# Kernel tuning notes

Hardware: AMD Instinct MI355X
Metric: run time of the kernel (lower is better)

The kernel has to match this reference:

```python
import jax, jax.numpy as jnp
import numpy as np

N0, N1, F, H = 30000, 6000, 1024, 512
E00, E01, E10, E11 = 600000, 300000, 300000, 400000


def setup_inputs() -> dict:
    key = jax.random.key(0)
    keys = iter(jax.random.split(key, 64))

    def randn(shape, s=1.0):
        return jax.random.normal(next(keys), shape, dtype=jnp.float32) * s

    inp = {"feat0": randn((N0, F)), "feat1": randn((N1, F))}
    adj_specs = {"a00": (N0, N0, E00), "a01": (N0, N1, E01),
                 "a10": (N1, N0, E10), "a11a": (N1, N1, E11), "a11b": (N1, N1, E11)}
    for name, (ni, nj, e) in adj_specs.items():
        inp[name + "_row"] = jax.random.randint(next(keys), (e,), 0, ni, dtype=jnp.int32)
        inp[name + "_col"] = jax.random.randint(next(keys), (e,), 0, nj, dtype=jnp.int32)
        inp[name + "_val"] = jax.random.uniform(next(keys), (e,), dtype=jnp.float32)
    for rel in ["00", "01", "10", "11a", "11b"]:
        inp["W1_" + rel] = randn((F, H), 0.02)
        inp["W2_" + rel] = randn((H, H), 0.05)
        inp["W3_" + rel] = randn((H, H), 0.05)
    return inp


def _spmm(row, col, val, x, n_out):
    # sparse adjacency (n_out x n_in) @ x, COO edge-list form
    return jax.ops.segment_sum(val[:, None] * x[col], row, num_segments=n_out)


def reference(feat0, feat1,
              a00_row, a00_col, a00_val, a01_row, a01_col, a01_val,
              a10_row, a10_col, a10_val, a11a_row, a11a_col, a11a_val,
              a11b_row, a11b_col, a11b_val,
              W1_00, W1_01, W1_10, W1_11a, W1_11b,
              W2_00, W2_01, W2_10, W2_11a, W2_11b,
              W3_00, W3_01, W3_10, W3_11a, W3_11b):
    relu = jax.nn.relu

    def conv(row, col, val, x, W, n_out):
        # GraphConvolution(Sparse)Multi with identity act: adj @ (x @ W)
        return _spmm(row, col, val, x @ W, n_out)

    # Layer 1: relu(add_n over (i, j) edge types)
    e0_0 = relu(conv(a00_row, a00_col, a00_val, feat0, W1_00, N0)
                + conv(a01_row, a01_col, a01_val, feat1, W1_01, N0))
    e0_1 = relu(conv(a10_row, a10_col, a10_val, feat0, W1_10, N1)
                + conv(a11a_row, a11a_col, a11a_val, feat1, W1_11a, N1)
                + conv(a11b_row, a11b_col, a11b_val, feat1, W1_11b, N1))

    # Layer 2: original does embeddings1 = embeddings0 + embeddings1 (python list
    # concat), so embeddings1[j] == embeddings0[j] -> layer-2 inputs are e0.
    e2_0 = relu(conv(a00_row, a00_col, a00_val, e0_0, W2_00, N0)
                + conv(a01_row, a01_col, a01_val, e0_1, W2_01, N0))
    e2_1 = relu(conv(a10_row, a10_col, a10_val, e0_0, W2_10, N1)
                + conv(a11a_row, a11a_col, a11a_val, e0_1, W2_11a, N1)
                + conv(a11b_row, a11b_col, a11b_val, e0_1, W2_11b, N1))

    # Layer 3: inputs are layer-2 outputs (same list-concat quirk); no relu.
    e3_0 = (conv(a00_row, a00_col, a00_val, e2_0, W3_00, N0)
            + conv(a01_row, a01_col, a01_val, e2_1, W3_01, N0))
    e3_1 = (conv(a10_row, a10_col, a10_val, e2_0, W3_10, N1)
            + conv(a11a_row, a11a_col, a11a_val, e2_1, W3_11a, N1)
            + conv(a11b_row, a11b_col, a11b_val, e2_1, W3_11b, N1))

    # Final: concat([e0, embeddings1(=e0), e3]) per object type; stack obj types
    # along node axis for a single output array.
    out0 = jnp.concatenate([e0_0, e0_0, e3_0], axis=1)  # [N0, 3H]
    out1 = jnp.concatenate([e0_1, e0_1, e3_1], axis=1)  # [N1, 3H]
    return jnp.concatenate([out0, out1], axis=0)  # [N0+N1, 3H]
```

## Files before the change

kernel.cpp:

```cpp
#include <hip/hip_runtime.h>
#include <stdint.h>

#define N0 30000
#define N1 6000
#define FDIM 1024
#define HDIM 512
#define E00 600000
#define E01 300000
#define E10 300000
#define E11A 400000
#define E11B 400000
#define NE_TOT (E00 + E01 + E10 + E11A + E11B)

typedef __attribute__((ext_vector_type(4))) float f32x4;
typedef __attribute__((ext_vector_type(8))) __bf16 bf16x8;

__device__ __forceinline__ unsigned short f2bf(float f) {
  unsigned u = __float_as_uint(f);
  u += 0x7fffu + ((u >> 16) & 1u);
  return (unsigned short)(u >> 16);
}

__device__ __forceinline__ void gload16(const void* g, void* l) {
  __builtin_amdgcn_global_load_lds((const __attribute__((address_space(1))) void*)g,
                                   (__attribute__((address_space(3))) void*)l, 16, 0, 0);
}

__global__ void conv_bf16_kernel(const float* __restrict__ src, unsigned short* __restrict__ dst, int n4) {
  int gid = blockIdx.x * blockDim.x + threadIdx.x;
  if (gid >= n4) return;
  float4 v = ((const float4*)src)[gid];
  ushort4 o;
  o.x = f2bf(v.x); o.y = f2bf(v.y); o.z = f2bf(v.z); o.w = f2bf(v.w);
  ((ushort4*)dst)[gid] = o;
}

__global__ void conv_weights_kernel(const float* __restrict__ w00, const float* __restrict__ w10,
                                    const float* __restrict__ w01, const float* __restrict__ w11a,
                                    const float* __restrict__ w11b,
                                    unsigned short* __restrict__ dst0, unsigned short* __restrict__ dst1, int K) {
  int gid = blockIdx.x * blockDim.x + threadIdx.x;
  int total0 = 1024 * K;
  int total1 = 1536 * K;
  if (gid < total0) {
    int n = gid / K, k = gid - n * K;
    const float* w = (n < 512) ? w00 : w10;
    int nn = n & 511;
    dst0[gid] = f2bf(w[(size_t)k * 512 + nn]);
  } else if (gid < total0 + total1) {
    int g = gid - total0;
    int n = g / K, k = g - n * K;
    const float* w = (n < 512) ? w01 : ((n < 1024) ? w11a : w11b);
    int nn = n & 511;
    dst1[g] = f2bf(w[(size_t)k * 512 + nn]);
  }
}

__global__ void zero_ints(int* p, int n) {
  int g = blockIdx.x * blockDim.x + threadIdx.x;
  if (g < n) p[g] = 0;
}

__global__ void hist5(const int* __restrict__ r0, const int* __restrict__ r1, const int* __restrict__ r2,
                      const int* __restrict__ r3, const int* __restrict__ r4,
                      int* c0, int* c1, int* c2, int* c3, int* c4) {
  int g = blockIdx.x * blockDim.x + threadIdx.x;
  const int* r; int* c; int e;
  if (g < E00) { r = r0; c = c0; e = g; }
  else if (g < E00 + E01) { r = r1; c = c1; e = g - E00; }
  else if (g < E00 + E01 + E10) { r = r2; c = c2; e = g - (E00 + E01); }
  else if (g < E00 + E01 + E10 + E11A) { r = r3; c = c3; e = g - (E00 + E01 + E10); }
  else if (g < NE_TOT) { r = r4; c = c4; e = g - (E00 + E01 + E10 + E11A); }
  else return;
  atomicAdd(&c[r[e]], 1);
}

__global__ __launch_bounds__(1024) void scan5p(int* c0, int* rp0, int* c1, int* rp1,
                                               int* c2, int* rp2, int* c3, int* rp3,
                                               int* c4, int* rp4) {
  int b = blockIdx.x;
  int* cnt; int* rp; int n;
  if (b == 0) { cnt = c0; rp = rp0; n = N0; }
  else if (b == 1) { cnt = c1; rp = rp1; n = N0; }
  else if (b == 2) { cnt = c2; rp = rp2; n = N1; }
  else if (b == 3) { cnt = c3; rp = rp3; n = N1; }
  else { cnt = c4; rp = rp4; n = N1; }
  __shared__ int wsum[16];
  const int tid = threadIdx.x, lane = tid & 63, w = tid >> 6;
  int carry = 0;
  for (int base = 0; base < n; base += 1024) {
    int i = base + tid;
    int v = (i < n) ? cnt[i] : 0;
    int x = v;
    #pragma unroll
    for (int d = 1; d < 64; d <<= 1) {
      int y = __shfl_up(x, d, 64);
      if (lane >= d) x += y;
    }
    if (lane == 63) wsum[w] = x;
    __syncthreads();
    if (w == 0) {
      int t = (lane < 16) ? wsum[lane] : 0;
      #pragma unroll
      for (int d = 1; d < 16; d <<= 1) {
        int y = __shfl_up(t, d, 64);
        if (lane >= d) t += y;
      }
      if (lane < 16) wsum[lane] = t;
    }
    __syncthreads();
    int wpref = (w > 0) ? wsum[w - 1] : 0;
    int excl = carry + wpref + (x - v);
    if (i < n) { rp[i] = excl; cnt[i] = excl; }
    carry += wsum[15];
    __syncthreads();
  }
  if (tid == 0) rp[n] = carry;
}

__global__ void scatter5(const int* __restrict__ r0, const int* __restrict__ q0, const float* __restrict__ v0,
                         int* cur0, int* sc0, float* sv0,
                         const int* __restrict__ r1, const int* __restrict__ q1, const float* __restrict__ v1,
                         int* cur1, int* sc1, float* sv1,
                         const int* __restrict__ r2, const int* __restrict__ q2, const float* __restrict__ v2,
                         int* cur2, int* sc2, float* sv2,
                         const int* __restrict__ r3, const int* __restrict__ q3, const float* __restrict__ v3,
                         int* cur3, int* sc3, float* sv3,
                         const int* __restrict__ r4, const int* __restrict__ q4, const float* __restrict__ v4,
                         int* cur4, int* sc4, float* sv4) {
  int g = blockIdx.x * blockDim.x + threadIdx.x;
  const int* r; const int* q; const float* v; int* cur; int* sc; float* sv; int e;
  if (g < E00) { r = r0; q = q0; v = v0; cur = cur0; sc = sc0; sv = sv0; e = g; }
  else if (g < E00 + E01) { r = r1; q = q1; v = v1; cur = cur1; sc = sc1; sv = sv1; e = g - E00; }
  else if (g < E00 + E01 + E10) { r = r2; q = q2; v = v2; cur = cur2; sc = sc2; sv = sv2; e = g - (E00 + E01); }
  else if (g < E00 + E01 + E10 + E11A) { r = r3; q = q3; v = v3; cur = cur3; sc = sc3; sv = sv3; e = g - (E00 + E01 + E10); }
  else if (g < NE_TOT) { r = r4; q = q4; v = v4; cur = cur4; sc = sc4; sv = sv4; e = g - (E00 + E01 + E10 + E11A); }
  else return;
  int row = r[e];
  int p = atomicAdd(&cur[row], 1);
  sc[p] = q[e];
  sv[p] = v[e];
}

#define BM 128
#define BN 128
#define BK 64

__global__ __launch_bounds__(256) void gemm_bf16(const unsigned short* __restrict__ A,
                                                 const unsigned short* __restrict__ Bt,
                                                 unsigned short* __restrict__ C,
                                                 int M, int N, int K, int nbx) {
  __shared__ unsigned short As[BM * BK];
  __shared__ unsigned short Bs[BN * BK];
  const int nwg = gridDim.x;
  const int orig = blockIdx.x;
  const int q = nwg >> 3, rr = nwg & 7;
  const int xcd = orig & 7, pos = orig >> 3;
  const int wg = (xcd < rr ? xcd * (q + 1) : rr * (q + 1) + (xcd - rr) * q) + pos;
  const int bx = wg % nbx;
  const int by = wg / nbx;

  const int tid = threadIdx.x;
  const int lane = tid & 63;
  const int wid = tid >> 6;
  const int m0 = bx * BM;
  const int n0 = by * BN;
  const int wm = (wid >> 1) * 64;
  const int wn = (wid & 1) * 64;

  f32x4 acc[4][4] = {};

  const int srow = wid * 32 + (lane >> 3);
  const int scol = (lane & 7) * 8;

  for (int k0 = 0; k0 < K; k0 += BK) {
    #pragma unroll
    for (int c = 0; c < 4; ++c) {
      int gr = m0 + srow + c * 8;
      if (gr > M - 1) gr = M - 1;
      gload16(A + (size_t)gr * K + k0 + scol, As + (wid * 32 + c * 8) * BK);
      int gn = n0 + srow + c * 8;
      gload16(Bt + (size_t)gn * K + k0 + scol, Bs + (wid * 32 + c * 8) * BK);
    }
    __syncthreads();
    #pragma unroll
    for (int ks = 0; ks < 2; ++ks) {
      bf16x8 af[4], bfr[4];
      #pragma unroll
      for (int i = 0; i < 4; i++)
        af[i] = *(const bf16x8*)(As + (wm + i * 16 + (lane & 15)) * BK + ks * 32 + (lane >> 4) * 8);
      #pragma unroll
      for (int j = 0; j < 4; j++)
        bfr[j] = *(const bf16x8*)(Bs + (wn + j * 16 + (lane & 15)) * BK + ks * 32 + (lane >> 4) * 8);
      #pragma unroll
      for (int i = 0; i < 4; i++)
        #pragma unroll
        for (int j = 0; j < 4; j++)
          acc[i][j] = __builtin_amdgcn_mfma_f32_16x16x32_bf16(af[i], bfr[j], acc[i][j], 0, 0, 0);
    }
    __syncthreads();
  }

  #pragma unroll
  for (int i = 0; i < 4; i++) {
    int rbase = m0 + wm + i * 16 + (lane >> 4) * 4;
    #pragma unroll
    for (int j = 0; j < 4; j++) {
      int col = n0 + wn + j * 16 + (lane & 15);
      #pragma unroll
      for (int r = 0; r < 4; r++) {
        int row = rbase + r;
        if (row < M) C[(size_t)row * N + col] = f2bf(acc[i][j][r]);
      }
    }
  }
}

__device__ __forceinline__ void acc8(float* acc, float v, uint4 u) {
  acc[0] += v * __uint_as_float(u.x << 16);
  acc[1] += v * __uint_as_float(u.x & 0xffff0000u);
  acc[2] += v * __uint_as_float(u.y << 16);
  acc[3] += v * __uint_as_float(u.y & 0xffff0000u);
  acc[4] += v * __uint_as_float(u.z << 16);
  acc[5] += v * __uint_as_float(u.z & 0xffff0000u);
  acc[6] += v * __uint_as_float(u.w << 16);
  acc[7] += v * __uint_as_float(u.w & 0xffff0000u);
}

__global__ __launch_bounds__(256) void spmm_kernel(
    int nrows, int nseg,
    const int* __restrict__ rp0, const int* __restrict__ ci0, const float* __restrict__ cv0,
    const unsigned short* __restrict__ g0, int ld0, int off0,
    const int* __restrict__ rp1, const int* __restrict__ ci1, const float* __restrict__ cv1,
    const unsigned short* __restrict__ g1, int ld1, int off1,
    const int* __restrict__ rp2, const int* __restrict__ ci2, const float* __restrict__ cv2,
    const unsigned short* __restrict__ g2, int ld2, int off2,
    int do_relu,
    unsigned short* __restrict__ ebf,
    float* __restrict__ outp, int out_row0, int out_col0, int dup) {
  const int lane = threadIdx.x & 63;
  const int r = blockIdx.x * 4 + (threadIdx.x >> 6);
  if (r >= nrows) return;
  float acc[8] = {0.f, 0.f, 0.f, 0.f, 0.f, 0.f, 0.f, 0.f};
  for (int s = 0; s < nseg; ++s) {
    const int* rp; const int* ci; const float* cv; const unsigned short* g; int ld, off;
    if (s == 0) { rp = rp0; ci = ci0; cv = cv0; g = g0; ld = ld0; off = off0; }
    else if (s == 1) { rp = rp1; ci = ci1; cv = cv1; g = g1; ld = ld1; off = off1; }
    else { rp = rp2; ci = ci2; cv = cv2; g = g2; ld = ld2; off = off2; }
    const unsigned short* gb = g + off + lane * 8;
    int e = rp[r], e1 = rp[r + 1];
    for (; e + 3 < e1; e += 4) {
      int ca = ci[e], cb = ci[e + 1], cc = ci[e + 2], cd = ci[e + 3];
      float va = cv[e], vb = cv[e + 1], vc = cv[e + 2], vd = cv[e + 3];
      uint4 ua = *(const uint4*)(gb + (size_t)ca * ld);
      uint4 ub = *(const uint4*)(gb + (size_t)cb * ld);
      uint4 uc = *(const uint4*)(gb + (size_t)cc * ld);
      uint4 ud = *(const uint4*)(gb + (size_t)cd * ld);
      acc8(acc, va, ua); acc8(acc, vb, ub); acc8(acc, vc, uc); acc8(acc, vd, ud);
    }
    for (; e < e1; ++e) {
      int c = ci[e];
      float v = cv[e];
      uint4 u = *(const uint4*)(gb + (size_t)c * ld);
      acc8(acc, v, u);
    }
  }
  if (do_relu) {
    #pragma unroll
    for (int i = 0; i < 8; i++) acc[i] = fmaxf(acc[i], 0.f);
  }
  if (ebf) {
    uint4 o;
    o.x = (unsigned)f2bf(acc[0]) | ((unsigned)f2bf(acc[1]) << 16);
    o.y = (unsigned)f2bf(acc[2]) | ((unsigned)f2bf(acc[3]) << 16);
    o.z = (unsigned)f2bf(acc[4]) | ((unsigned)f2bf(acc[5]) << 16);
    o.w = (unsigned)f2bf(acc[6]) | ((unsigned)f2bf(acc[7]) << 16);
    *(uint4*)(ebf + (size_t)r * HDIM + lane * 8) = o;
  }
  if (outp) {
    float4 v0; v0.x = acc[0]; v0.y = acc[1]; v0.z = acc[2]; v0.w = acc[3];
    float4 v1; v1.x = acc[4]; v1.y = acc[5]; v1.z = acc[6]; v1.w = acc[7];
    size_t base = (size_t)(out_row0 + r) * 1536 + out_col0 + lane * 8;
    *(float4*)(outp + base) = v0;
    *(float4*)(outp + base + 4) = v1;
    if (dup) {
      *(float4*)(outp + base + 512) = v0;
      *(float4*)(outp + base + 516) = v1;
    }
  }
}

extern "C" void kernel_launch(void* const* d_in, const int* in_sizes, int n_in,
                              void* d_out, int out_size, void* d_ws, size_t ws_size,
                              hipStream_t stream) {
  const float* feat0 = (const float*)d_in[0];
  const float* feat1 = (const float*)d_in[1];
  const int* a00_row = (const int*)d_in[2];
  const int* a00_col = (const int*)d_in[3];
  const float* a00_val = (const float*)d_in[4];
  const int* a01_row = (const int*)d_in[5];
  const int* a01_col = (const int*)d_in[6];
  const float* a01_val = (const float*)d_in[7];
  const int* a10_row = (const int*)d_in[8];
  const int* a10_col = (const int*)d_in[9];
  const float* a10_val = (const float*)d_in[10];
  const int* a11a_row = (const int*)d_in[11];
  const int* a11a_col = (const int*)d_in[12];
  const float* a11a_val = (const float*)d_in[13];
  const int* a11b_row = (const int*)d_in[14];
  const int* a11b_col = (const int*)d_in[15];
  const float* a11b_val = (const float*)d_in[16];

  const float *W1[5], *W2[5], *W3[5];
  if (in_sizes[18] == 512 * 512) {
    for (int r = 0; r < 5; r++) {
      W1[r] = (const float*)d_in[17 + 3 * r];
      W2[r] = (const float*)d_in[18 + 3 * r];
      W3[r] = (const float*)d_in[19 + 3 * r];
    }
  } else {
    for (int r = 0; r < 5; r++) {
      W1[r] = (const float*)d_in[17 + r];
      W2[r] = (const float*)d_in[22 + r];
      W3[r] = (const float*)d_in[27 + r];
    }
  }

  char* ws = (char*)d_ws;
  size_t off = 0;
  auto alloc = [&](size_t bytes) -> char* {
    char* p = ws + off;
    off += (bytes + 255) & ~(size_t)255;
    return p;
  };
  unsigned short* feat0b = (unsigned short*)alloc((size_t)N0 * FDIM * 2);
  unsigned short* feat1b = (unsigned short*)alloc((size_t)N1 * FDIM * 2);
  unsigned short* Wt1_0 = (unsigned short*)alloc((size_t)1024 * 1024 * 2);
  unsigned short* Wt1_1 = (unsigned short*)alloc((size_t)1536 * 1024 * 2);
  unsigned short* Wt2_0 = (unsigned short*)alloc((size_t)1024 * 512 * 2);
  unsigned short* Wt2_1 = (unsigned short*)alloc((size_t)1536 * 512 * 2);
  unsigned short* Wt3_0 = (unsigned short*)alloc((size_t)1024 * 512 * 2);
  unsigned short* Wt3_1 = (unsigned short*)alloc((size_t)1536 * 512 * 2);
  unsigned short* G0 = (unsigned short*)alloc((size_t)N0 * 1024 * 2);
  unsigned short* G1 = (unsigned short*)alloc((size_t)N1 * 1536 * 2);
  unsigned short* e0_0 = (unsigned short*)alloc((size_t)N0 * HDIM * 2);
  unsigned short* e0_1 = (unsigned short*)alloc((size_t)N1 * HDIM * 2);
  int* cur = (int*)alloc((size_t)(2 * N0 + 3 * N1) * 4);
  int* cur00 = cur;
  int* cur01 = cur + N0;
  int* cur10 = cur + 2 * N0;
  int* cur11a = cur + 2 * N0 + N1;
  int* cur11b = cur + 2 * N0 + 2 * N1;
  int* rp00 = (int*)alloc((N0 + 1) * 4);
  int* rp01 = (int*)alloc((N0 + 1) * 4);
  int* rp10 = (int*)alloc((N1 + 1) * 4);
  int* rp11a = (int*)alloc((N1 + 1) * 4);
  int* rp11b = (int*)alloc((N1 + 1) * 4);
  int* sc00 = (int*)alloc((size_t)E00 * 4);
  float* sv00 = (float*)alloc((size_t)E00 * 4);
  int* sc01 = (int*)alloc((size_t)E01 * 4);
  float* sv01 = (float*)alloc((size_t)E01 * 4);
  int* sc10 = (int*)alloc((size_t)E10 * 4);
  float* sv10 = (float*)alloc((size_t)E10 * 4);
  int* sc11a = (int*)alloc((size_t)E11A * 4);
  float* sv11a = (float*)alloc((size_t)E11A * 4);
  int* sc11b = (int*)alloc((size_t)E11B * 4);
  float* sv11b = (float*)alloc((size_t)E11B * 4);
  unsigned short* e2_0 = feat0b;
  unsigned short* e2_1 = feat1b;
  float* out = (float*)d_out;

  conv_bf16_kernel<<<(N0 * FDIM / 4 + 255) / 256, 256, 0, stream>>>(feat0, feat0b, N0 * FDIM / 4);
  conv_bf16_kernel<<<(N1 * FDIM / 4 + 255) / 256, 256, 0, stream>>>(feat1, feat1b, N1 * FDIM / 4);
  conv_weights_kernel<<<(2560 * 1024 + 255) / 256, 256, 0, stream>>>(W1[0], W1[2], W1[1], W1[3], W1[4], Wt1_0, Wt1_1, 1024);
  conv_weights_kernel<<<(2560 * 512 + 255) / 256, 256, 0, stream>>>(W2[0], W2[2], W2[1], W2[3], W2[4], Wt2_0, Wt2_1, 512);
  conv_weights_kernel<<<(2560 * 512 + 255) / 256, 256, 0, stream>>>(W3[0], W3[2], W3[1], W3[3], W3[4], Wt3_0, Wt3_1, 512);

  int ncur = 2 * N0 + 3 * N1;
  zero_ints<<<(ncur + 255) / 256, 256, 0, stream>>>(cur, ncur);
  hist5<<<(NE_TOT + 255) / 256, 256, 0, stream>>>(a00_row, a01_row, a10_row, a11a_row, a11b_row,
                                                  cur00, cur01, cur10, cur11a, cur11b);
  scan5p<<<5, 1024, 0, stream>>>(cur00, rp00, cur01, rp01, cur10, rp10, cur11a, rp11a, cur11b, rp11b);
  scatter5<<<(NE_TOT + 255) / 256, 256, 0, stream>>>(
      a00_row, a00_col, a00_val, cur00, sc00, sv00,
      a01_row, a01_col, a01_val, cur01, sc01, sv01,
      a10_row, a10_col, a10_val, cur10, sc10, sv10,
      a11a_row, a11a_col, a11a_val, cur11a, sc11a, sv11a,
      a11b_row, a11b_col, a11b_val, cur11b, sc11b, sv11b);

  dim3 blk(256);
  int nbx0 = (N0 + BM - 1) / BM;
  int nbx1 = (N1 + BM - 1) / BM;
  dim3 g0a(nbx0 * (1024 / BN));
  dim3 g0b(nbx1 * (1536 / BN));

  gemm_bf16<<<g0a, blk, 0, stream>>>(feat0b, Wt1_0, G0, N0, 1024, 1024, nbx0);
  gemm_bf16<<<g0b, blk, 0, stream>>>(feat1b, Wt1_1, G1, N1, 1536, 1024, nbx1);
  spmm_kernel<<<(N0 + 3) / 4, blk, 0, stream>>>(N0, 2,
      rp00, sc00, sv00, G0, 1024, 0,
      rp01, sc01, sv01, G1, 1536, 0,
      nullptr, nullptr, nullptr, nullptr, 0, 0,
      1, e0_0, out, 0, 0, 1);
  spmm_kernel<<<(N1 + 3) / 4, blk, 0, stream>>>(N1, 3,
      rp10, sc10, sv10, G0, 1024, 512,
      rp11a, sc11a, sv11a, G1, 1536, 512,
      rp11b, sc11b, sv11b, G1, 1536, 1024,
      1, e0_1, out, N0, 0, 1);

  gemm_bf16<<<g0a, blk, 0, stream>>>(e0_0, Wt2_0, G0, N0, 1024, 512, nbx0);
  gemm_bf16<<<g0b, blk, 0, stream>>>(e0_1, Wt2_1, G1, N1, 1536, 512, nbx1);
  spmm_kernel<<<(N0 + 3) / 4, blk, 0, stream>>>(N0, 2,
      rp00, sc00, sv00, G0, 1024, 0,
      rp01, sc01, sv01, G1, 1536, 0,
      nullptr, nullptr, nullptr, nullptr, 0, 0,
      1, e2_0, nullptr, 0, 0, 0);
  spmm_kernel<<<(N1 + 3) / 4, blk, 0, stream>>>(N1, 3,
      rp10, sc10, sv10, G0, 1024, 512,
      rp11a, sc11a, sv11a, G1, 1536, 512,
      rp11b, sc11b, sv11b, G1, 1536, 1024,
      1, e2_1, nullptr, 0, 0, 0);

  gemm_bf16<<<g0a, blk, 0, stream>>>(e2_0, Wt3_0, G0, N0, 1024, 512, nbx0);
  gemm_bf16<<<g0b, blk, 0, stream>>>(e2_1, Wt3_1, G1, N1, 1536, 512, nbx1);
  spmm_kernel<<<(N0 + 3) / 4, blk, 0, stream>>>(N0, 2,
      rp00, sc00, sv00, G0, 1024, 0,
      rp01, sc01, sv01, G1, 1536, 0,
      nullptr, nullptr, nullptr, nullptr, 0, 0,
      0, nullptr, out, 0, 1024, 0);
  spmm_kernel<<<(N1 + 3) / 4, blk, 0, stream>>>(N1, 3,
      rp10, sc10, sv10, G0, 1024, 512,
      rp11a, sc11a, sv11a, G1, 1536, 512,
      rp11b, sc11b, sv11b, G1, 1536, 1024,
      0, nullptr, out, N0, 1024, 0);
}
```

Before: 1.347 ms.

## Reorder layers 2-3 to aggregate first, then multiply by concatenated weights

Layers 2 and 3 now compute (A·X) first for each relation, writing the aggregated features side by side into a wide buffer, and then run one GEMM with K-concatenated weights (K=1024 or 1536, N=512). This replaces the earlier (X·W) then SpMM order. The SpMM now gathers 512-wide rows instead of slices of 1024/1536-wide rows, and the per-relation sums fold into the GEMM's K reduction. ReLU and the fp32 output write are fused into the GEMM epilogue. The gather loop is also unrolled to 8 edges, and row bounds are made wave-uniform with readfirstlane.

```diff
diff --git a/kernel.cpp b/kernel.cpp
--- a/kernel.cpp
+++ b/kernel.cpp
@@ -53,6 +53,25 @@
     const float* w = (n < 512) ? w01 : ((n < 1024) ? w11a : w11b);
     int nn = n & 511;
     dst1[g] = f2bf(w[(size_t)k * 512 + nn]);
+  }
+}
+
+__global__ void conv_wk_kernel(const float* __restrict__ w00, const float* __restrict__ w01,
+                               const float* __restrict__ w10, const float* __restrict__ w11a,
+                               const float* __restrict__ w11b,
+                               unsigned short* __restrict__ dst0, unsigned short* __restrict__ dst1) {
+  int gid = blockIdx.x * blockDim.x + threadIdx.x;
+  const int T0 = 512 * 1024;
+  const int T1 = 512 * 1536;
+  if (gid < T0) {
+    int n = gid >> 10, k = gid & 1023;
+    const float* w = (k < 512) ? w00 : w01;
+    dst0[gid] = f2bf(w[(size_t)(k & 511) * 512 + n]);
+  } else if (gid < T0 + T1) {
+    int g = gid - T0;
+    int n = g / 1536, k = g - n * 1536;
+    const float* w = (k < 512) ? w10 : ((k < 1024) ? w11a : w11b);
+    dst1[g] = f2bf(w[(size_t)(k & 511) * 512 + n]);
   }
 }
 
@@ -146,10 +165,11 @@
 #define BN 128
 #define BK 64
 
+template<int MODE>
 __global__ __launch_bounds__(256) void gemm_bf16(const unsigned short* __restrict__ A,
                                                  const unsigned short* __restrict__ Bt,
-                                                 unsigned short* __restrict__ C,
-                                                 int M, int N, int K, int nbx) {
+                                                 void* __restrict__ Cv,
+                                                 int M, int N, int K, int nbx, int ldc) {
   __shared__ unsigned short As[BM * BK];
   __shared__ unsigned short Bs[BN * BK];
   const int nwg = gridDim.x;
@@ -210,13 +230,18 @@
       #pragma unroll
       for (int r = 0; r < 4; r++) {
         int row = rbase + r;
-        if (row < M) C[(size_t)row * N + col] = f2bf(acc[i][j][r]);
+        if (row < M) {
+          float v = acc[i][j][r];
+          if (MODE == 1) v = fmaxf(v, 0.f);
+          if (MODE == 2) ((float*)Cv)[(size_t)row * ldc + col] = v;
+          else ((unsigned short*)Cv)[(size_t)row * ldc + col] = f2bf(v);
+        }
       }
     }
   }
 }
 
-__device__ __forceinline__ void acc8(float* acc, float v, uint4 u) {
+__device__ __forceinline__ void acc8(float* acc, float v, const uint4& u) {
   acc[0] += v * __uint_as_float(u.x << 16);
   acc[1] += v * __uint_as_float(u.x & 0xffff0000u);
   acc[2] += v * __uint_as_float(u.y << 16);
@@ -227,6 +252,33 @@
   acc[7] += v * __uint_as_float(u.w & 0xffff0000u);
 }
 
+__device__ __forceinline__ void gather_row(const int* __restrict__ ci, const float* __restrict__ cv,
+                                           const unsigned short* __restrict__ gb, int ld,
+                                           int e, int e1, float* acc) {
+  for (; e + 7 < e1; e += 8) {
+    int c0 = ci[e], c1 = ci[e + 1], c2 = ci[e + 2], c3 = ci[e + 3];
+    int c4 = ci[e + 4], c5 = ci[e + 5], c6 = ci[e + 6], c7 = ci[e + 7];
+    float v0 = cv[e], v1 = cv[e + 1], v2 = cv[e + 2], v3 = cv[e + 3];
+    float v4 = cv[e + 4], v5 = cv[e + 5], v6 = cv[e + 6], v7 = cv[e + 7];
+    uint4 u0 = *(const uint4*)(gb + (size_t)c0 * ld);
+    uint4 u1 = *(const uint4*)(gb + (size_t)c1 * ld);
+    uint4 u2 = *(const uint4*)(gb + (size_t)c2 * ld);
+    uint4 u3 = *(const uint4*)(gb + (size_t)c3 * ld);
+    uint4 u4 = *(const uint4*)(gb + (size_t)c4 * ld);
+    uint4 u5 = *(const uint4*)(gb + (size_t)c5 * ld);
+    uint4 u6 = *(const uint4*)(gb + (size_t)c6 * ld);
+    uint4 u7 = *(const uint4*)(gb + (size_t)c7 * ld);
+    acc8(acc, v0, u0); acc8(acc, v1, u1); acc8(acc, v2, u2); acc8(acc, v3, u3);
+    acc8(acc, v4, u4); acc8(acc, v5, u5); acc8(acc, v6, u6); acc8(acc, v7, u7);
+  }
+  for (; e < e1; ++e) {
+    int c = ci[e];
+    float v = cv[e];
+    uint4 u = *(const uint4*)(gb + (size_t)c * ld);
+    acc8(acc, v, u);
+  }
+}
+
 __global__ __launch_bounds__(256) void spmm_kernel(
     int nrows, int nseg,
     const int* __restrict__ rp0, const int* __restrict__ ci0, const float* __restrict__ cv0,
@@ -235,9 +287,8 @@
     const unsigned short* __restrict__ g1, int ld1, int off1,
     const int* __restrict__ rp2, const int* __restrict__ ci2, const float* __restrict__ cv2,
     const unsigned short* __restrict__ g2, int ld2, int off2,
-    int do_relu,
     unsigned short* __restrict__ ebf,
-    float* __restrict__ outp, int out_row0, int out_col0, int dup) {
+    float* __restrict__ outp, int out_row0) {
   const int lane = threadIdx.x & 63;
   const int r = blockIdx.x * 4 + (threadIdx.x >> 6);
   if (r >= nrows) return;
@@ -247,46 +298,54 @@
     if (s == 0) { rp = rp0; ci = ci0; cv = cv0; g = g0; ld = ld0; off = off0; }
     else if (s == 1) { rp = rp1; ci = ci1; cv = cv1; g = g1; ld = ld1; off = off1; }
     else { rp = rp2; ci = ci2; cv = cv2; g = g2; ld = ld2; off = off2; }
-    const unsigned short* gb = g + off + lane * 8;
-    int e = rp[r], e1 = rp[r + 1];
-    for (; e + 3 < e1; e += 4) {
-      int ca = ci[e], cb = ci[e + 1], cc = ci[e + 2], cd = ci[e + 3];
-      float va = cv[e], vb = cv[e + 1], vc = cv[e + 2], vd = cv[e + 3];
-      uint4 ua = *(const uint4*)(gb + (size_t)ca * ld);
-      uint4 ub = *(const uint4*)(gb + (size_t)cb * ld);
-      uint4 uc = *(const uint4*)(gb + (size_t)cc * ld);
-      uint4 ud = *(const uint4*)(gb + (size_t)cd * ld);
-      acc8(acc, va, ua); acc8(acc, vb, ub); acc8(acc, vc, uc); acc8(acc, vd, ud);
-    }
-    for (; e < e1; ++e) {
-      int c = ci[e];
-      float v = cv[e];
-      uint4 u = *(const uint4*)(gb + (size_t)c * ld);
-      acc8(acc, v, u);
-    }
-  }
-  if (do_relu) {
-    #pragma unroll
-    for (int i = 0; i < 8; i++) acc[i] = fmaxf(acc[i], 0.f);
-  }
-  if (ebf) {
+    int e = __builtin_amdgcn_readfirstlane(rp[r]);
+    int e1 = __builtin_amdgcn_readfirstlane(rp[r + 1]);
+    gather_row(ci, cv, g + off + lane * 8, ld, e, e1, acc);
+  }
+  #pragma unroll
+  for (int i = 0; i < 8; i++) acc[i] = fmaxf(acc[i], 0.f);
+  uint4 o;
+  o.x = (unsigned)f2bf(acc[0]) | ((unsigned)f2bf(acc[1]) << 16);
+  o.y = (unsigned)f2bf(acc[2]) | ((unsigned)f2bf(acc[3]) << 16);
+  o.z = (unsigned)f2bf(acc[4]) | ((unsigned)f2bf(acc[5]) << 16);
+  o.w = (unsigned)f2bf(acc[6]) | ((unsigned)f2bf(acc[7]) << 16);
+  *(uint4*)(ebf + (size_t)r * HDIM + lane * 8) = o;
+  float4 v0; v0.x = acc[0]; v0.y = acc[1]; v0.z = acc[2]; v0.w = acc[3];
+  float4 v1; v1.x = acc[4]; v1.y = acc[5]; v1.z = acc[6]; v1.w = acc[7];
+  size_t base = (size_t)(out_row0 + r) * 1536 + lane * 8;
+  *(float4*)(outp + base) = v0;
+  *(float4*)(outp + base + 4) = v1;
+  *(float4*)(outp + base + 512) = v0;
+  *(float4*)(outp + base + 516) = v1;
+}
+
+__global__ __launch_bounds__(256) void spmm_sep(
+    int nrows, int nseg,
+    const int* __restrict__ rp0, const int* __restrict__ ci0, const float* __restrict__ cv0,
+    const unsigned short* __restrict__ t0,
+    const int* __restrict__ rp1, const int* __restrict__ ci1, const float* __restrict__ cv1,
+    const unsigned short* __restrict__ t1,
+    const int* __restrict__ rp2, const int* __restrict__ ci2, const float* __restrict__ cv2,
+    const unsigned short* __restrict__ t2,
+    unsigned short* __restrict__ outp, int ld_out) {
+  const int lane = threadIdx.x & 63;
+  const int r = blockIdx.x * 4 + (threadIdx.x >> 6);
+  if (r >= nrows) return;
+  for (int s = 0; s < nseg; ++s) {
+    const int* rp; const int* ci; const float* cv; const unsigned short* t;
+    if (s == 0) { rp = rp0; ci = ci0; cv = cv0; t = t0; }
+    else if (s == 1) { rp = rp1; ci = ci1; cv = cv1; t = t1; }
+    else { rp = rp2; ci = ci2; cv = cv2; t = t2; }
+    float acc[8] = {0.f, 0.f, 0.f, 0.f, 0.f, 0.f, 0.f, 0.f};
+    int e = __builtin_amdgcn_readfirstlane(rp[r]);
+    int e1 = __builtin_amdgcn_readfirstlane(rp[r + 1]);
+    gather_row(ci, cv, t + lane * 8, HDIM, e, e1, acc);
     uint4 o;
     o.x = (unsigned)f2bf(acc[0]) | ((unsigned)f2bf(acc[1]) << 16);
     o.y = (unsigned)f2bf(acc[2]) | ((unsigned)f2bf(acc[3]) << 16);
     o.z = (unsigned)f2bf(acc[4]) | ((unsigned)f2bf(acc[5]) << 16);
     o.w = (unsigned)f2bf(acc[6]) | ((unsigned)f2bf(acc[7]) << 16);
-    *(uint4*)(ebf + (size_t)r * HDIM + lane * 8) = o;
-  }
-  if (outp) {
-    float4 v0; v0.x = acc[0]; v0.y = acc[1]; v0.z = acc[2]; v0.w = acc[3];
-    float4 v1; v1.x = acc[4]; v1.y = acc[5]; v1.z = acc[6]; v1.w = acc[7];
-    size_t base = (size_t)(out_row0 + r) * 1536 + out_col0 + lane * 8;
-    *(float4*)(outp + base) = v0;
-    *(float4*)(outp + base + 4) = v1;
-    if (dup) {
-      *(float4*)(outp + base + 512) = v0;
-      *(float4*)(outp + base + 516) = v1;
-    }
+    *(uint4*)(outp + (size_t)r * ld_out + s * HDIM + lane * 8) = o;
   }
 }
 
@@ -337,10 +396,10 @@
   unsigned short* feat1b = (unsigned short*)alloc((size_t)N1 * FDIM * 2);
   unsigned short* Wt1_0 = (unsigned short*)alloc((size_t)1024 * 1024 * 2);
   unsigned short* Wt1_1 = (unsigned short*)alloc((size_t)1536 * 1024 * 2);
-  unsigned short* Wt2_0 = (unsigned short*)alloc((size_t)1024 * 512 * 2);
-  unsigned short* Wt2_1 = (unsigned short*)alloc((size_t)1536 * 512 * 2);
-  unsigned short* Wt3_0 = (unsigned short*)alloc((size_t)1024 * 512 * 2);
-  unsigned short* Wt3_1 = (unsigned short*)alloc((size_t)1536 * 512 * 2);
+  unsigned short* Wt2_0 = (unsigned short*)alloc((size_t)512 * 1024 * 2);
+  unsigned short* Wt2_1 = (unsigned short*)alloc((size_t)512 * 1536 * 2);
+  unsigned short* Wt3_0 = (unsigned short*)alloc((size_t)512 * 1024 * 2);
+  unsigned short* Wt3_1 = (unsigned short*)alloc((size_t)512 * 1536 * 2);
   unsigned short* G0 = (unsigned short*)alloc((size_t)N0 * 1024 * 2);
   unsigned short* G1 = (unsigned short*)alloc((size_t)N1 * 1536 * 2);
   unsigned short* e0_0 = (unsigned short*)alloc((size_t)N0 * HDIM * 2);
@@ -373,8 +432,8 @@
   conv_bf16_kernel<<<(N0 * FDIM / 4 + 255) / 256, 256, 0, stream>>>(feat0, feat0b, N0 * FDIM / 4);
   conv_bf16_kernel<<<(N1 * FDIM / 4 + 255) / 256, 256, 0, stream>>>(feat1, feat1b, N1 * FDIM / 4);
   conv_weights_kernel<<<(2560 * 1024 + 255) / 256, 256, 0, stream>>>(W1[0], W1[2], W1[1], W1[3], W1[4], Wt1_0, Wt1_1, 1024);
-  conv_weights_kernel<<<(2560 * 512 + 255) / 256, 256, 0, stream>>>(W2[0], W2[2], W2[1], W2[3], W2[4], Wt2_0, Wt2_1, 512);
-  conv_weights_kernel<<<(2560 * 512 + 255) / 256, 256, 0, stream>>>(W3[0], W3[2], W3[1], W3[3], W3[4], Wt3_0, Wt3_1, 512);
+  conv_wk_kernel<<<(512 * 2560 + 255) / 256, 256, 0, stream>>>(W2[0], W2[1], W2[2], W2[3], W2[4], Wt2_0, Wt2_1);
+  conv_wk_kernel<<<(512 * 2560 + 255) / 256, 256, 0, stream>>>(W3[0], W3[1], W3[2], W3[3], W3[4], Wt3_0, Wt3_1);
 
   int ncur = 2 * N0 + 3 * N1;
   zero_ints<<<(ncur + 255) / 256, 256, 0, stream>>>(cur, ncur);
@@ -391,45 +450,43 @@
   dim3 blk(256);
   int nbx0 = (N0 + BM - 1) / BM;
   int nbx1 = (N1 + BM - 1) / BM;
-  dim3 g0a(nbx0 * (1024 / BN));
-  dim3 g0b(nbx1 * (1536 / BN));
-
-  gemm_bf16<<<g0a, blk, 0, stream>>>(feat0b, Wt1_0, G0, N0, 1024, 1024, nbx0);
-  gemm_bf16<<<g0b, blk, 0, stream>>>(feat1b, Wt1_1, G1, N1, 1536, 1024, nbx1);
+
+  gemm_bf16<0><<<dim3(nbx0 * 8), blk, 0, stream>>>(feat0b, Wt1_0, G0, N0, 1024, 1024, nbx0, 1024);
+  gemm_bf16<0><<<dim3(nbx1 * 12), blk, 0, stream>>>(feat1b, Wt1_1, G1, N1, 1536, 1024, nbx1, 1536);
   spmm_kernel<<<(N0 + 3) / 4, blk, 0, stream>>>(N0, 2,
       rp00, sc00, sv00, G0, 1024, 0,
       rp01, sc01, sv01, G1, 1536, 0,
       nullptr, nullptr, nullptr, nullptr, 0, 0,
-      1, e0_0, out, 0, 0, 1);
+      e0_0, out, 0);
   spmm_kernel<<<(N1 + 3) / 4, blk, 0, stream>>>(N1, 3,
       rp10, sc10, sv10, G0, 1024, 512,
       rp11a, sc11a, sv11a, G1, 1536, 512,
       rp11b, sc11b, sv11b, G1, 1536, 1024,
-      1, e0_1, out, N0, 0, 1);
-
-  gemm_bf16<<<g0a, blk, 0, stream>>>(e0_0, Wt2_0, G0, N0, 1024, 512, nbx0);
-  gemm_bf16<<<g0b, blk, 0, stream>>>(e0_1, Wt2_1, G1, N1, 1536, 512, nbx1);
-  spmm_kernel<<<(N0 + 3) / 4, blk, 0, stream>>>(N0, 2,
-      rp00, sc00, sv00, G0, 1024, 0,
-      rp01, sc01, sv01, G1, 1536, 0,
-      nullptr, nullptr, nullptr, nullptr, 0, 0,
-      1, e2_0, nullptr, 0, 0, 0);
-  spmm_kernel<<<(N1 + 3) / 4, blk, 0, stream>>>(N1, 3,
-      rp10, sc10, sv10, G0, 1024, 512,
-      rp11a, sc11a, sv11a, G1, 1536, 512,
-      rp11b, sc11b, sv11b, G1, 1536, 1024,
-      1, e2_1, nullptr, 0, 0, 0);
-
-  gemm_bf16<<<g0a, blk, 0, stream>>>(e2_0, Wt3_0, G0, N0, 1024, 512, nbx0);
-  gemm_bf16<<<g0b, blk, 0, stream>>>(e2_1, Wt3_1, G1, N1, 1536, 512, nbx1);
-  spmm_kernel<<<(N0 + 3) / 4, blk, 0, stream>>>(N0, 2,
-      rp00, sc00, sv00, G0, 1024, 0,
-      rp01, sc01, sv01, G1, 1536, 0,
-      nullptr, nullptr, nullptr, nullptr, 0, 0,
-      0, nullptr, out, 0, 1024, 0);
-  spmm_kernel<<<(N1 + 3) / 4, blk, 0, stream>>>(N1, 3,
-      rp10, sc10, sv10, G0, 1024, 512,
-      rp11a, sc11a, sv11a, G1, 1536, 512,
-      rp11b, sc11b, sv11b, G1, 1536, 1024,
-      0, nullptr, out, N0, 1024, 0);
-}
+      e0_1, out, N0);
+
+  spmm_sep<<<(N0 + 3) / 4, blk, 0, stream>>>(N0, 2,
+      rp00, sc00, sv00, e0_0,
+      rp01, sc01, sv01, e0_1,
+      nullptr, nullptr, nullptr, nullptr,
+      G0, 1024);
+  spmm_sep<<<(N1 + 3) / 4, blk, 0, stream>>>(N1, 3,
+      rp10, sc10, sv10, e0_0,
+      rp11a, sc11a, sv11a, e0_1,
+      rp11b, sc11b, sv11b, e0_1,
+      G1, 1536);
+  gemm_bf16<1><<<dim3(nbx0 * 4), blk, 0, stream>>>(G0, Wt2_0, e2_0, N0, 512, 1024, nbx0, 512);
+  gemm_bf16<1><<<dim3(nbx1 * 4), blk, 0, stream>>>(G1, Wt2_1, e2_1, N1, 512, 1536, nbx1, 512);
+
+  spmm_sep<<<(N0 + 3) / 4, blk, 0, stream>>>(N0, 2,
+      rp00, sc00, sv00, e2_0,
+      rp01, sc01, sv01, e2_1,
+      nullptr, nullptr, nullptr, nullptr,
+      G0, 1024);
+  spmm_sep<<<(N1 + 3) / 4, blk, 0, stream>>>(N1, 3,
+      rp10, sc10, sv10, e2_0,
+      rp11a, sc11a, sv11a, e2_1,
+      rp11b, sc11b, sv11b, e2_1,
+      G1, 1536);
+  gemm_bf16<2><<<dim3(nbx0 * 4), blk, 0, stream>>>(G0, Wt3_0, out + 1024, N0, 512, 1024, nbx0, 1536);
+  gemm_bf16<2><<<dim3(nbx1 * 4), blk, 0, stream>>>(G1, Wt3_1, out + (size_t)N0 * 1536 + 1024, N1, 512, 1536, nbx1, 1536);
+}
```

New measurement: 1.376 ms. 2.1% more time.
